# Optimization experiments

Hardware: AMD Instinct MI355X
Metric: run time of the kernel (lower is better)

## Reference

```python
import jax, jax.numpy as jnp
import numpy as np

N_NODES = 100000
N_EDGES = 1600000
N_GRAPHS = 256
IN_FEATS = 64
H_FEATS = 128
GN_EPS = 1e-5


def setup_inputs() -> dict:
    key = jax.random.key(0)
    ks = jax.random.split(key, 8)
    inputs = jax.random.normal(ks[0], (N_NODES, IN_FEATS), dtype=jnp.float32)
    edge_index = jax.random.randint(ks[1], (2, N_EDGES), 0, N_NODES, dtype=jnp.int64)
    batch = jnp.sort(jax.random.randint(ks[2], (N_NODES,), 0, N_GRAPHS, dtype=jnp.int64))
    edge_attr = jax.random.normal(ks[3], (N_EDGES, 8), dtype=jnp.float32)
    W1 = jax.random.normal(ks[4], (IN_FEATS, H_FEATS), dtype=jnp.float32) * 0.05
    W2 = jax.random.normal(ks[5], (H_FEATS, H_FEATS), dtype=jnp.float32) * 0.05
    W3 = jax.random.normal(ks[6], (H_FEATS, H_FEATS), dtype=jnp.float32) * 0.05
    return {
        'inputs': inputs, 'edge_index': edge_index, 'batch': batch, 'edge_attr': edge_attr,
        'W1': W1, 'b1': jnp.zeros((H_FEATS,), jnp.float32),
        'W2': W2, 'b2': jnp.zeros((H_FEATS,), jnp.float32),
        'W3': W3, 'b3': jnp.zeros((H_FEATS,), jnp.float32),
        'gn_weight': jnp.ones((H_FEATS,), jnp.float32),
        'gn_bias': jnp.zeros((H_FEATS,), jnp.float32),
        'gn_mean_scale': jnp.ones((H_FEATS,), jnp.float32),
    }


def reference(inputs, edge_index, batch, edge_attr, W1, b1, W2, b2, W3, b3, gn_weight, gn_bias, gn_mean_scale):
    src, dst = edge_index[0], edge_index[1]
    # GINConv with eps=0: h_i = MLP((1+eps)*x_i + sum_{j in N(i)} x_j)
    agg = jax.ops.segment_sum(inputs[src], dst, num_segments=N_NODES)
    h = inputs + agg
    # 3-layer ReLU MLP
    h = jax.nn.relu(h @ W1 + b1)
    h = jax.nn.relu(h @ W2 + b2)
    h = jax.nn.relu(h @ W3 + b3)
    # GraphNorm (per-graph mean shift with learnable mean_scale, then per-graph rms normalize)
    cnt = jnp.maximum(jax.ops.segment_sum(jnp.ones((N_NODES, 1), h.dtype), batch, num_segments=N_GRAPHS), 1.0)
    mean = jax.ops.segment_sum(h, batch, num_segments=N_GRAPHS) / cnt  # [G, H]
    out = h - mean[batch] * gn_mean_scale
    var = jax.ops.segment_sum(out * out, batch, num_segments=N_GRAPHS) / cnt  # [G, H]
    h_emb = out / jnp.sqrt(var[batch] + GN_EPS) * gn_weight + gn_bias
    # add_residue=False -> plain ReLU
    h_emb = jax.nn.relu(h_emb)
    # global max pool over each graph segment
    flat = jax.ops.segment_max(h_emb, batch, num_segments=N_GRAPHS)
    return (h_emb, flat, edge_index, edge_attr, batch)
```

## Files before the change

### kernel.cpp

```cpp
#include <hip/hip_runtime.h>
#include <math.h>

#define N_NODES 100000
#define N_EDGES 1600000
#define N_GRAPHS 256
#define IN_F 64
#define H_F 128
#define GN_EPS 1e-5f
#define PAD 32
#define NBINS 8
#define LCAP 512
#define BINCAP (1 << 18)
#define NSUB 16
#define SUBW 782
#define SBCAP 16384
#define MG 782
#define CPB 1612
#define CP_EI4 800000
#define CP_TOT 825000

typedef __attribute__((ext_vector_type(8))) short bf16x8;
typedef __attribute__((ext_vector_type(4))) float f32x4;

__device__ __forceinline__ float bf2f(unsigned short u) {
  return __uint_as_float(((unsigned int)u) << 16);
}
__device__ __forceinline__ unsigned short f2bf(float f) {
  unsigned int u = __float_as_uint(f);
  u += 0x7FFFu + ((u >> 16) & 1u);
  return (unsigned short)(u >> 16);
}
__device__ __forceinline__ int bsearch_batch(const int* __restrict__ batch, int target) {
  int lo = 0, hi = N_NODES;
  while (lo < hi) { int mid = (lo + hi) >> 1; if (batch[mid] < target) lo = mid + 1; else hi = mid; }
  return lo;
}

#define PREP_XH   1600000
#define PREP_GS   (PREP_XH + 16384)
#define PREP_WT   (PREP_GS + 40960)
#define PREP_CTR  (PREP_WT + 40)
#define PREP_FL   (PREP_CTR + 8192)
__global__ __launch_bounds__(256) void k_prep(
    const float4* __restrict__ xin, const float* __restrict__ W1,
    const float* __restrict__ W2, const float* __restrict__ W3,
    ushort4* __restrict__ xh4, float4* __restrict__ gsum4,
    unsigned short* __restrict__ wt, int4* __restrict__ ctr4,
    float4* __restrict__ flat4) {
  int i = blockIdx.x * 256 + threadIdx.x;
  if (i < PREP_XH) {
    float4 v = xin[i];
    ushort4 o;
    o.x = f2bf(v.x); o.y = f2bf(v.y); o.z = f2bf(v.z); o.w = f2bf(v.w);
    xh4[i] = o;
  } else if (i < PREP_GS) {
    gsum4[i - PREP_XH] = make_float4(0.f, 0.f, 0.f, 0.f);
  } else if (i < PREP_WT) {
    int j = i - PREP_GS;
    if (j < 8192) {
      int n = j >> 6, k = j & 63;
      wt[j] = f2bf(W1[(size_t)k * H_F + n]);
    } else if (j < 24576) {
      int jj = j - 8192;
      int n = jj >> 7, k = jj & 127;
      wt[j] = f2bf(W2[(size_t)k * H_F + n]);
    } else {
      int jj = j - 24576;
      int n = jj >> 7, k = jj & 127;
      wt[j] = f2bf(W3[(size_t)k * H_F + n]);
    }
  } else if (i < PREP_CTR) {
    ctr4[i - PREP_WT] = make_int4(0, 0, 0, 0);
  } else if (i < PREP_FL) {
    flat4[i - PREP_CTR] = make_float4(-INFINITY, -INFINITY, -INFINITY, -INFINITY);
  }
}

__global__ __launch_bounds__(256) void k_bin(
    const int* __restrict__ src, const int* __restrict__ dst,
    unsigned int* __restrict__ binBuf, int* __restrict__ gbc) {
  __shared__ unsigned int ebuf[NBINS][LCAP];
  __shared__ int lcnt[NBINS];
  __shared__ int lbase[NBINS];
  const int t = threadIdx.x;
  if (t < NBINS) lcnt[t] = 0;
  __syncthreads();
  for (int e0 = blockIdx.x * 256; e0 < N_EDGES; e0 += gridDim.x * 256) {
    int e = e0 + t;
    if (e < N_EDGES) {
      int s = src[e], d = dst[e];
      int b = d / 12500;
      int p = atomicAdd(&lcnt[b], 1);
      ebuf[b][p] = ((unsigned)(d - b * 12500) << 17) | (unsigned)s;
    }
    __syncthreads();
    if (t < NBINS && lcnt[t] >= 256) lbase[t] = atomicAdd(&gbc[t], lcnt[t]);
    __syncthreads();
#pragma unroll
    for (int b = 0; b < NBINS; ++b) {
      int c = lcnt[b];
      if (c >= 256) {
        unsigned int* gp = binBuf + (size_t)b * BINCAP + lbase[b];
        for (int i = t; i < c; i += 256) gp[i] = ebuf[b][i];
      }
    }
    __syncthreads();
    if (t < NBINS && lcnt[t] >= 256) lcnt[t] = 0;
    __syncthreads();
  }
  if (t < NBINS && lcnt[t] > 0) lbase[t] = atomicAdd(&gbc[t], lcnt[t]);
  __syncthreads();
#pragma unroll
  for (int b = 0; b < NBINS; ++b) {
    int c = lcnt[b];
    if (c > 0) {
      unsigned int* gp = binBuf + (size_t)b * BINCAP + lbase[b];
      for (int i = t; i < c; i += 256) gp[i] = ebuf[b][i];
    }
  }
}

__global__ __launch_bounds__(256) void k_bin2(
    const unsigned int* __restrict__ binBuf, const int* __restrict__ gbc,
    unsigned int* __restrict__ binBuf2, int* __restrict__ gbc2) {
  __shared__ unsigned int ebuf[NSUB][LCAP];
  __shared__ int lcnt[NSUB];
  __shared__ int lbase[NSUB];
  const int t = threadIdx.x;
  const int p = blockIdx.x & 7;
  const int blk = blockIdx.x >> 3;
  const int nb = gbc[p];
  const unsigned int* buf = binBuf + (size_t)p * BINCAP;
  if (t < NSUB) lcnt[t] = 0;
  __syncthreads();
  for (int i0 = blk * 256; i0 < nb; i0 += 32 * 256) {
    int i = i0 + t;
    if (i < nb) {
      unsigned int e = buf[i];
      int dloc = (int)(e >> 17);
      int sub = dloc / SUBW;
      int p2 = atomicAdd(&lcnt[sub], 1);
      ebuf[sub][p2] = ((unsigned)(dloc - sub * SUBW) << 17) | (e & 131071u);
    }
    __syncthreads();
    if (t < NSUB && lcnt[t] >= 256)
      lbase[t] = atomicAdd(&gbc2[p * NSUB + t], lcnt[t]);
    __syncthreads();
#pragma unroll
    for (int b = 0; b < NSUB; ++b) {
      int c = lcnt[b];
      if (c >= 256) {
        unsigned int* gp = binBuf2 + (size_t)(p * NSUB + b) * SBCAP + lbase[b];
        for (int i2 = t; i2 < c; i2 += 256) gp[i2] = ebuf[b][i2];
      }
    }
    __syncthreads();
    if (t < NSUB && lcnt[t] >= 256) lcnt[t] = 0;
    __syncthreads();
  }
  if (t < NSUB && lcnt[t] > 0)
    lbase[t] = atomicAdd(&gbc2[p * NSUB + t], lcnt[t]);
  __syncthreads();
#pragma unroll
  for (int b = 0; b < NSUB; ++b) {
    int c = lcnt[b];
    if (c > 0) {
      unsigned int* gp = binBuf2 + (size_t)(p * NSUB + b) * SBCAP + lbase[b];
      for (int i2 = t; i2 < c; i2 += 256) gp[i2] = ebuf[b][i2];
    }
  }
}

__global__ __launch_bounds__(256) void k_fill5(
    const unsigned int* __restrict__ binBuf2, const int* __restrict__ gbc2,
    int* __restrict__ csr, int* __restrict__ cnt,
    int* __restrict__ ovfc, int* __restrict__ ovf) {
  __shared__ int lcsr[SUBW * PAD];
  __shared__ int lcnt[SUBW];
  const int t = threadIdx.x;
  const int p = blockIdx.x & 7;
  const int sub = blockIdx.x >> 3;
  for (int j = t; j < SUBW; j += 256) lcnt[j] = 0;
  __syncthreads();
  const int n2 = gbc2[p * NSUB + sub];
  const unsigned int* buf = binBuf2 + (size_t)(p * NSUB + sub) * SBCAP;
  const int dbase = p * 12500 + sub * SUBW;
  for (int i = t; i < n2; i += 256) {
    unsigned int e = buf[i];
    int dloc2 = (int)(e >> 17);
    int s = (int)(e & 131071u);
    int pos = atomicAdd(&lcnt[dloc2], 1);
    if (pos < PAD) {
      lcsr[dloc2 * PAD + pos] = s;
    } else {
      int o = atomicAdd(ovfc, 1);
      ovf[2 * o] = s;
      ovf[2 * o + 1] = dbase + dloc2;
    }
  }
  __syncthreads();
  int rows = 12500 - sub * SUBW; if (rows > SUBW) rows = SUBW;
  int total4 = rows * (PAD / 4);
  int4* dst4 = (int4*)(csr + (size_t)dbase * PAD);
  const int4* src4 = (const int4*)lcsr;
  for (int i = t; i < total4; i += 256) dst4[i] = src4[i];
  for (int j = t; j < rows; j += 256)
    cnt[dbase + j] = lcnt[j];
}

__global__ __launch_bounds__(256) void k_gather(
    const unsigned short* __restrict__ xh, const int* __restrict__ csr,
    const int* __restrict__ cnt, unsigned short* __restrict__ xa,
    const int* __restrict__ ovfc, const int* __restrict__ ovf) {
  int wid = (blockIdx.x * 256 + threadIdx.x) >> 6;
  if (wid >= N_NODES) return;
  const int lane = threadIdx.x & 63;
  const int g = lane >> 4;
  const int fl = lane & 15;
  int rawdeg = cnt[wid];
  int deg = rawdeg > PAD ? PAD : rawdeg;
  int myE = csr[(size_t)wid * PAD + (lane & 31)];
  float s0 = 0.f, s1 = 0.f, s2 = 0.f, s3 = 0.f;
  int j = g;
  for (; j + 12 < deg; j += 16) {
    int sA = __shfl(myE, j);
    int sB = __shfl(myE, j + 4);
    int sC = __shfl(myE, j + 8);
    int sD = __shfl(myE, j + 12);
    ushort4 a = *(const ushort4*)&xh[(size_t)sA * IN_F + fl * 4];
    ushort4 b = *(const ushort4*)&xh[(size_t)sB * IN_F + fl * 4];
    ushort4 c = *(const ushort4*)&xh[(size_t)sC * IN_F + fl * 4];
    ushort4 d = *(const ushort4*)&xh[(size_t)sD * IN_F + fl * 4];
    s0 += bf2f(a.x) + bf2f(b.x) + bf2f(c.x) + bf2f(d.x);
    s1 += bf2f(a.y) + bf2f(b.y) + bf2f(c.y) + bf2f(d.y);
    s2 += bf2f(a.z) + bf2f(b.z) + bf2f(c.z) + bf2f(d.z);
    s3 += bf2f(a.w) + bf2f(b.w) + bf2f(c.w) + bf2f(d.w);
  }
  for (; j < deg; j += 4) {
    int sA = __shfl(myE, j);
    ushort4 a = *(const ushort4*)&xh[(size_t)sA * IN_F + fl * 4];
    s0 += bf2f(a.x); s1 += bf2f(a.y); s2 += bf2f(a.z); s3 += bf2f(a.w);
  }
  if (rawdeg > PAD && g == 0) {
    int n = *ovfc;
    for (int o = 0; o < n; ++o) {
      if (ovf[2 * o + 1] == wid) {
        int s = ovf[2 * o];
        ushort4 a = *(const ushort4*)&xh[(size_t)s * IN_F + fl * 4];
        s0 += bf2f(a.x); s1 += bf2f(a.y); s2 += bf2f(a.z); s3 += bf2f(a.w);
      }
    }
  }
  s0 += __shfl_xor(s0, 16); s1 += __shfl_xor(s1, 16);
  s2 += __shfl_xor(s2, 16); s3 += __shfl_xor(s3, 16);
  s0 += __shfl_xor(s0, 32); s1 += __shfl_xor(s1, 32);
  s2 += __shfl_xor(s2, 32); s3 += __shfl_xor(s3, 32);
  if (g == 0) {
    ushort4 self = *(const ushort4*)&xh[(size_t)wid * IN_F + fl * 4];
    s0 += bf2f(self.x); s1 += bf2f(self.y);
    s2 += bf2f(self.z); s3 += bf2f(self.w);
    ushort4 r;
    r.x = f2bf(s0); r.y = f2bf(s1); r.z = f2bf(s2); r.w = f2bf(s3);
    *(ushort4*)&xa[(size_t)wid * IN_F + fl * 4] = r;
  }
}

__global__ __launch_bounds__(512) void k_mlp(
    const unsigned short* __restrict__ xa,
    const unsigned short* __restrict__ wt1,
    const unsigned short* __restrict__ wt2,
    const unsigned short* __restrict__ wt3,
    const float* __restrict__ b1, const float* __restrict__ b2,
    const float* __restrict__ b3,
    unsigned short* __restrict__ h3,
    const int* __restrict__ batch,
    float* __restrict__ gsum, float* __restrict__ gsumq,
    const int4* __restrict__ ei4, const int4* __restrict__ bat4,
    float4* __restrict__ o_ei4, float4* __restrict__ o_b4) {
  __shared__ unsigned short sh[128 * 128];
  __shared__ float ssum[H_F], ssq[H_F];
  const int t = threadIdx.x;
  if (blockIdx.x >= MG) {
    int cb = blockIdx.x - MG;
    for (int i = cb * 512 + t; i < CP_TOT; i += CPB * 512) {
      if (i < CP_EI4) {
        int4 v = ei4[i];
        o_ei4[i] = make_float4((float)v.x, (float)v.y, (float)v.z, (float)v.w);
      } else {
        int j = i - CP_EI4;
        int4 v = bat4[j];
        o_b4[j] = make_float4((float)v.x, (float)v.y, (float)v.z, (float)v.w);
      }
    }
    return;
  }
  const int lane = t & 63;
  const int wv = t >> 6;
  const int row16 = lane & 15;
  const int kg = lane >> 4;
  const long blk0 = (long)blockIdx.x * 128;
  const int lr0 = (wv & 3) * 32;
  const int nb = (wv >> 2) * 4;
  f32x4 acc0[4], acc1[4];

  {
    long arow0 = blk0 + lr0 + row16;      if (arow0 > N_NODES - 1) arow0 = N_NODES - 1;
    long arow1 = blk0 + lr0 + 16 + row16; if (arow1 > N_NODES - 1) arow1 = N_NODES - 1;
    bf16x8 a0[2], a1[2];
    const unsigned short* ap0 = xa + arow0 * IN_F + kg * 8;
    const unsigned short* ap1 = xa + arow1 * IN_F + kg * 8;
#pragma unroll
    for (int s = 0; s < 2; ++s) {
      a0[s] = *(const bf16x8*)(ap0 + s * 32);
      a1[s] = *(const bf16x8*)(ap1 + s * 32);
    }
#pragma unroll
    for (int n = 0; n < 4; ++n) {
      acc0[n] = (f32x4){0.f, 0.f, 0.f, 0.f};
      acc1[n] = (f32x4){0.f, 0.f, 0.f, 0.f};
    }
#pragma unroll
    for (int n = 0; n < 4; ++n) {
      const unsigned short* wpn =
          wt1 + (size_t)((nb + n) * 16 + row16) * IN_F + kg * 8;
      bf16x8 b[2];
      b[0] = *(const bf16x8*)(wpn);
      b[1] = *(const bf16x8*)(wpn + 32);
      acc0[n] = __builtin_amdgcn_mfma_f32_16x16x32_bf16(a0[0], b[0], acc0[n], 0, 0, 0);
      acc0[n] = __builtin_amdgcn_mfma_f32_16x16x32_bf16(a0[1], b[1], acc0[n], 0, 0, 0);
      acc1[n] = __builtin_amdgcn_mfma_f32_16x16x32_bf16(a1[0], b[0], acc1[n], 0, 0, 0);
      acc1[n] = __builtin_amdgcn_mfma_f32_16x16x32_bf16(a1[1], b[1], acc1[n], 0, 0, 0);
    }
#pragma unroll
    for (int n = 0; n < 4; ++n) {
      int col = (nb + n) * 16 + row16;
      float bv = b1[col];
#pragma unroll
      for (int r = 0; r < 4; ++r) {
        int lrow0 = lr0 + kg * 4 + r;
        int lrow1 = lrow0 + 16;
        sh[lrow0 * 128 + (col ^ ((lrow0 & 7) << 3))] = f2bf(fmaxf(acc0[n][r] + bv, 0.f));
        sh[lrow1 * 128 + (col ^ ((lrow1 & 7) << 3))] = f2bf(fmaxf(acc1[n][r] + bv, 0.f));
      }
    }
  }
  __syncthreads();

  {
    const int lA0 = lr0 + row16, lA1 = lr0 + 16 + row16;
    bf16x8 a0[4], a1[4];
#pragma unroll
    for (int s = 0; s < 4; ++s) {
      int K0 = s * 32 + kg * 8;
      a0[s] = *(const bf16x8*)&sh[lA0 * 128 + (K0 ^ ((lA0 & 7) << 3))];
      a1[s] = *(const bf16x8*)&sh[lA1 * 128 + (K0 ^ ((lA1 & 7) << 3))];
    }
#pragma unroll
    for (int n = 0; n < 4; ++n) {
      acc0[n] = (f32x4){0.f, 0.f, 0.f, 0.f};
      acc1[n] = (f32x4){0.f, 0.f, 0.f, 0.f};
    }
#pragma unroll
    for (int n = 0; n < 4; ++n) {
      const unsigned short* wpn =
          wt2 + (size_t)((nb + n) * 16 + row16) * H_F + kg * 8;
      bf16x8 b[4];
#pragma unroll
      for (int s = 0; s < 4; ++s) b[s] = *(const bf16x8*)(wpn + s * 32);
#pragma unroll
      for (int s = 0; s < 4; ++s) {
        acc0[n] = __builtin_amdgcn_mfma_f32_16x16x32_bf16(a0[s], b[s], acc0[n], 0, 0, 0);
        acc1[n] = __builtin_amdgcn_mfma_f32_16x16x32_bf16(a1[s], b[s], acc1[n], 0, 0, 0);
      }
    }
    __syncthreads();
#pragma unroll
    for (int n = 0; n < 4; ++n) {
      int col = (nb + n) * 16 + row16;
      float bv = b2[col];
#pragma unroll
      for (int r = 0; r < 4; ++r) {
        int lrow0 = lr0 + kg * 4 + r;
        int lrow1 = lrow0 + 16;
        sh[lrow0 * 128 + (col ^ ((lrow0 & 7) << 3))] = f2bf(fmaxf(acc0[n][r] + bv, 0.f));
        sh[lrow1 * 128 + (col ^ ((lrow1 & 7) << 3))] = f2bf(fmaxf(acc1[n][r] + bv, 0.f));
      }
    }
  }
  __syncthreads();

  {
    const int lA0 = lr0 + row16, lA1 = lr0 + 16 + row16;
    bf16x8 a0[4], a1[4];
#pragma unroll
    for (int s = 0; s < 4; ++s) {
      int K0 = s * 32 + kg * 8;
      a0[s] = *(const bf16x8*)&sh[lA0 * 128 + (K0 ^ ((lA0 & 7) << 3))];
      a1[s] = *(const bf16x8*)&sh[lA1 * 128 + (K0 ^ ((lA1 & 7) << 3))];
    }
#pragma unroll
    for (int n = 0; n < 4; ++n) {
      acc0[n] = (f32x4){0.f, 0.f, 0.f, 0.f};
      acc1[n] = (f32x4){0.f, 0.f, 0.f, 0.f};
    }
#pragma unroll
    for (int n = 0; n < 4; ++n) {
      const unsigned short* wpn =
          wt3 + (size_t)((nb + n) * 16 + row16) * H_F + kg * 8;
      bf16x8 b[4];
#pragma unroll
      for (int s = 0; s < 4; ++s) b[s] = *(const bf16x8*)(wpn + s * 32);
#pragma unroll
      for (int s = 0; s < 4; ++s) {
        acc0[n] = __builtin_amdgcn_mfma_f32_16x16x32_bf16(a0[s], b[s], acc0[n], 0, 0, 0);
        acc1[n] = __builtin_amdgcn_mfma_f32_16x16x32_bf16(a1[s], b[s], acc1[n], 0, 0, 0);
      }
    }
#pragma unroll
    for (int n = 0; n < 4; ++n) {
      int col = (nb + n) * 16 + row16;
      float bv = b3[col];
#pragma unroll
      for (int r = 0; r < 4; ++r) {
        long row0 = blk0 + lr0 + kg * 4 + r;
        long row1 = row0 + 16;
        if (row0 < N_NODES)
          h3[row0 * H_F + col] = f2bf(fmaxf(acc0[n][r] + bv, 0.f));
        if (row1 < N_NODES)
          h3[row1 * H_F + col] = f2bf(fmaxf(acc1[n][r] + bv, 0.f));
      }
    }
    long lastrow = blk0 + 127; if (lastrow > N_NODES - 1) lastrow = N_NODES - 1;
    const int glo = batch[blk0];
    const int ghi = batch[lastrow];
    int br0[4], br1[4];
#pragma unroll
    for (int r = 0; r < 4; ++r) {
      long row0 = blk0 + lr0 + kg * 4 + r;
      long row1 = row0 + 16;
      br0[r] = (row0 < N_NODES) ? batch[row0] : -1;
      br1[r] = (row1 < N_NODES) ? batch[row1] : -1;
    }
    for (int g = glo; g <= ghi; ++g) {
      if (t < H_F) { ssum[t] = 0.f; ssq[t] = 0.f; }
      __syncthreads();
#pragma unroll
      for (int n = 0; n < 4; ++n) {
        int col = (nb + n) * 16 + row16;
        float bvn = b3[col];
        float sn = 0.f, qn = 0.f;
#pragma unroll
        for (int r = 0; r < 4; ++r) {
          if (br0[r] == g) { float f = fmaxf(acc0[n][r] + bvn, 0.f); sn += f; qn += f * f; }
          if (br1[r] == g) { float f = fmaxf(acc1[n][r] + bvn, 0.f); sn += f; qn += f * f; }
        }
        sn += __shfl_xor(sn, 16); qn += __shfl_xor(qn, 16);
        sn += __shfl_xor(sn, 32); qn += __shfl_xor(qn, 32);
        if (kg == 0) {
          atomicAdd(&ssum[col], sn);
          atomicAdd(&ssq[col], qn);
        }
      }
      __syncthreads();
      if (t < H_F) {
        unsafeAtomicAdd(&gsum[(size_t)g * H_F + t], ssum[t]);
        unsafeAtomicAdd(&gsumq[(size_t)g * H_F + t], ssq[t]);
      }
      __syncthreads();
    }
  }
}

__global__ __launch_bounds__(256) void k_apply2(
    const unsigned short* __restrict__ h3, const int* __restrict__ batch,
    const float* __restrict__ gsum, const float* __restrict__ gsumsq,
    const float* __restrict__ gms, const float* __restrict__ gw,
    const float* __restrict__ gb, float* __restrict__ hemb,
    float* __restrict__ flat) {
  const int t = threadIdx.x;
  const int rg = t >> 5, fq = t & 31;
  const int m0 = blockIdx.x * 32;
  const int r0 = m0 + rg * 4;
  const int c0 = fq * 4;
  const float4 bb = *(const float4*)&gb[c0];
  const float4 gm = *(const float4*)&gms[c0];
  const float4 gwv = *(const float4*)&gw[c0];
  const int glo = batch[m0], ghi = batch[m0 + 31];
  __shared__ int sb[2];
  __shared__ __align__(16) float4 mred[8][32];
  if (glo == ghi) {
    if (t < 2) sb[t] = bsearch_batch(batch, glo + t);
    __syncthreads();
    float c = fmaxf((float)(sb[1] - sb[0]), 1.0f);
    float4 S = *(const float4*)&gsum[(size_t)glo * H_F + c0];
    float4 Q = *(const float4*)&gsumsq[(size_t)glo * H_F + c0];
    float4 mm, ss;
    {
      float mean, ms, var;
      mean = S.x / c; ms = mean * gm.x; var = fmaxf(Q.x / c - 2.f * ms * mean + ms * ms, 0.f);
      mm.x = ms; ss.x = gwv.x * rsqrtf(var + GN_EPS);
      mean = S.y / c; ms = mean * gm.y; var = fmaxf(Q.y / c - 2.f * ms * mean + ms * ms, 0.f);
      mm.y = ms; ss.y = gwv.y * rsqrtf(var + GN_EPS);
      mean = S.z / c; ms = mean * gm.z; var = fmaxf(Q.z / c - 2.f * ms * mean + ms * ms, 0.f);
      mm.z = ms; ss.z = gwv.z * rsqrtf(var + GN_EPS);
      mean = S.w / c; ms = mean * gm.w; var = fmaxf(Q.w / c - 2.f * ms * mean + ms * ms, 0.f);
      mm.w = ms; ss.w = gwv.w * rsqrtf(var + GN_EPS);
    }
    float4 mx = {-INFINITY, -INFINITY, -INFINITY, -INFINITY};
#pragma unroll
    for (int i = 0; i < 4; ++i) {
      size_t idx = (size_t)(r0 + i) * H_F + c0;
      ushort4 u = *(const ushort4*)&h3[idx];
      float4 v;
      v.x = fmaxf((bf2f(u.x) - mm.x) * ss.x + bb.x, 0.f);
      v.y = fmaxf((bf2f(u.y) - mm.y) * ss.y + bb.y, 0.f);
      v.z = fmaxf((bf2f(u.z) - mm.z) * ss.z + bb.z, 0.f);
      v.w = fmaxf((bf2f(u.w) - mm.w) * ss.w + bb.w, 0.f);
      *(float4*)&hemb[idx] = v;
      mx.x = fmaxf(mx.x, v.x); mx.y = fmaxf(mx.y, v.y);
      mx.z = fmaxf(mx.z, v.z); mx.w = fmaxf(mx.w, v.w);
    }
    mred[rg][fq] = mx;
    __syncthreads();
    if (rg == 0) {
#pragma unroll
      for (int j = 1; j < 8; ++j) {
        float4 a = mred[j][fq];
        mx.x = fmaxf(mx.x, a.x); mx.y = fmaxf(mx.y, a.y);
        mx.z = fmaxf(mx.z, a.z); mx.w = fmaxf(mx.w, a.w);
      }
      int* pf = (int*)&flat[(size_t)glo * H_F + c0];
      atomicMax(pf + 0, __float_as_int(mx.x));
      atomicMax(pf + 1, __float_as_int(mx.y));
      atomicMax(pf + 2, __float_as_int(mx.z));
      atomicMax(pf + 3, __float_as_int(mx.w));
    }
  } else {
    int gcur = -1;
    float4 mm = {0,0,0,0}, ss = {0,0,0,0};
    float4 mx = {-INFINITY, -INFINITY, -INFINITY, -INFINITY};
#pragma unroll
    for (int i = 0; i < 4; ++i) {
      int g = batch[r0 + i];
      if (g != gcur) {
        if (gcur >= 0) {
          int* pf = (int*)&flat[(size_t)gcur * H_F + c0];
          atomicMax(pf + 0, __float_as_int(mx.x));
          atomicMax(pf + 1, __float_as_int(mx.y));
          atomicMax(pf + 2, __float_as_int(mx.z));
          atomicMax(pf + 3, __float_as_int(mx.w));
          mx = make_float4(-INFINITY, -INFINITY, -INFINITY, -INFINITY);
        }
        gcur = g;
        int lo = bsearch_batch(batch, g);
        int hi = bsearch_batch(batch, g + 1);
        float c = fmaxf((float)(hi - lo), 1.0f);
        float4 S = *(const float4*)&gsum[(size_t)g * H_F + c0];
        float4 Q = *(const float4*)&gsumsq[(size_t)g * H_F + c0];
        float mean, ms, var;
        mean = S.x / c; ms = mean * gm.x; var = fmaxf(Q.x / c - 2.f * ms * mean + ms * ms, 0.f);
        mm.x = ms; ss.x = gwv.x * rsqrtf(var + GN_EPS);
        mean = S.y / c; ms = mean * gm.y; var = fmaxf(Q.y / c - 2.f * ms * mean + ms * ms, 0.f);
        mm.y = ms; ss.y = gwv.y * rsqrtf(var + GN_EPS);
        mean = S.z / c; ms = mean * gm.z; var = fmaxf(Q.z / c - 2.f * ms * mean + ms * ms, 0.f);
        mm.z = ms; ss.z = gwv.z * rsqrtf(var + GN_EPS);
        mean = S.w / c; ms = mean * gm.w; var = fmaxf(Q.w / c - 2.f * ms * mean + ms * ms, 0.f);
        mm.w = ms; ss.w = gwv.w * rsqrtf(var + GN_EPS);
      }
      size_t idx = (size_t)(r0 + i) * H_F + c0;
      ushort4 u = *(const ushort4*)&h3[idx];
      float4 v;
      v.x = fmaxf((bf2f(u.x) - mm.x) * ss.x + bb.x, 0.f);
      v.y = fmaxf((bf2f(u.y) - mm.y) * ss.y + bb.y, 0.f);
      v.z = fmaxf((bf2f(u.z) - mm.z) * ss.z + bb.z, 0.f);
      v.w = fmaxf((bf2f(u.w) - mm.w) * ss.w + bb.w, 0.f);
      *(float4*)&hemb[idx] = v;
      mx.x = fmaxf(mx.x, v.x); mx.y = fmaxf(mx.y, v.y);
      mx.z = fmaxf(mx.z, v.z); mx.w = fmaxf(mx.w, v.w);
    }
    int* pf = (int*)&flat[(size_t)gcur * H_F + c0];
    atomicMax(pf + 0, __float_as_int(mx.x));
    atomicMax(pf + 1, __float_as_int(mx.y));
    atomicMax(pf + 2, __float_as_int(mx.z));
    atomicMax(pf + 3, __float_as_int(mx.w));
  }
}

__global__ __launch_bounds__(256) void k_copy_ea(
    const float4* __restrict__ ea4, float4* __restrict__ o_ea4, int n4) {
  int i = blockIdx.x * 256 + threadIdx.x;
  if (i < n4) o_ea4[i] = ea4[i];
}

extern "C" void kernel_launch(void* const* d_in, const int* in_sizes, int n_in,
                              void* d_out, int out_size, void* d_ws, size_t ws_size,
                              hipStream_t stream) {
  const float* inputs = (const float*)d_in[0];
  const int*   ei     = (const int*)d_in[1];
  const int*   batch  = (const int*)d_in[2];
  const float* eattr  = (const float*)d_in[3];
  const float* W1 = (const float*)d_in[4];
  const float* b1 = (const float*)d_in[5];
  const float* W2 = (const float*)d_in[6];
  const float* b2 = (const float*)d_in[7];
  const float* W3 = (const float*)d_in[8];
  const float* b3 = (const float*)d_in[9];
  const float* gw  = (const float*)d_in[10];
  const float* gb  = (const float*)d_in[11];
  const float* gms = (const float*)d_in[12];

  float* out = (float*)d_out;
  float* hemb  = out;
  float* flat  = out + 12800000;
  float* o_ei  = out + 12832768;
  float* o_ea  = out + 16032768;
  float* o_b   = out + 28832768;

  unsigned int*   binBuf  = (unsigned int*)hemb;
  unsigned int*   binBuf2 = (unsigned int*)(hemb + 2100000);
  unsigned short* xh = (unsigned short*)(hemb + 4200000);
  unsigned short* xa = (unsigned short*)(hemb + 7600000);
  int*            csr = (int*)o_ea;
  unsigned short* h3  = (unsigned short*)(o_ea + 6400000);
  float* gsum  = o_ea + 3200000;
  float* gsumq = o_ea + 3232768;
  unsigned short* wt  = (unsigned short*)(o_ea + 3265536);
  unsigned short* wt1 = wt;
  unsigned short* wt2 = wt + 8192;
  unsigned short* wt3 = wt + 24576;
  int*   cnt   = (int*)o_ei;
  int*   ovfc  = (int*)o_ei + 100000;
  int*   gbc   = (int*)o_ei + 100008;
  int*   gbc2  = (int*)o_ei + 100016;
  int*   ovf   = (int*)o_ei + 100160;

  k_prep<<<(PREP_FL + 255) / 256, 256, 0, stream>>>(
      (const float4*)inputs, W1, W2, W3, (ushort4*)xh, (float4*)gsum, wt,
      (int4*)ovfc, (float4*)flat);
  k_bin<<<512, 256, 0, stream>>>(ei, ei + N_EDGES, binBuf, gbc);
  k_bin2<<<256, 256, 0, stream>>>(binBuf, gbc, binBuf2, gbc2);
  k_fill5<<<NBINS * NSUB, 256, 0, stream>>>(binBuf2, gbc2, csr, cnt, ovfc, ovf);
  k_gather<<<(N_NODES * 64 + 255) / 256, 256, 0, stream>>>(xh, csr, cnt, xa, ovfc, ovf);
  k_mlp<<<MG + CPB, 512, 0, stream>>>(xa, wt1, wt2, wt3, b1, b2, b3, h3, batch,
                                      gsum, gsumq, (const int4*)ei,
                                      (const int4*)batch, (float4*)o_ei,
                                      (float4*)o_b);
  k_apply2<<<N_NODES / 32, 256, 0, stream>>>(h3, batch, gsum, gsumq, gms, gw, gb,
                                             hemb, flat);
  k_copy_ea<<<(N_EDGES * 2 + 255) / 256, 256, 0, stream>>>(
      (const float4*)eattr, (float4*)o_ea, N_EDGES * 2);
}
```

Before: 245.4 us.

## Move scratch to workspace and overlap output copies with gather and MLP

When the workspace is large enough, h3 moves into the workspace and the CSR count/overflow buffers move into the edge_attr output region. This frees the edge_index and batch output regions, so their int-to-float conversion can run in extra blocks of the gather kernel. The edge_attr copy then runs inside spare MLP blocks instead of a separate full-size kernel, and a small kernel afterwards copies only the window still used by gsum/weights. The aim is to hide output copy bandwidth behind compute kernels, at the cost of a more complex buffer aliasing scheme that depends on ws_size.

```diff
diff --git a/kernel.cpp b/kernel.cpp
--- a/kernel.cpp
+++ b/kernel.cpp
@@ -16,8 +16,13 @@
 #define SBCAP 16384
 #define MG 782
 #define CPB 1612
+#define GCB 25000
+#define GCPB 1000
 #define CP_EI4 800000
-#define CP_TOT 825000
+#define CP_EIB 825000
+#define EA_TOT4 3200000
+#define WIN_LO 800000
+#define WIN_HI 821504
 
 typedef __attribute__((ext_vector_type(8))) short bf16x8;
 typedef __attribute__((ext_vector_type(4))) float f32x4;
@@ -211,7 +216,24 @@
 __global__ __launch_bounds__(256) void k_gather(
     const unsigned short* __restrict__ xh, const int* __restrict__ csr,
     const int* __restrict__ cnt, unsigned short* __restrict__ xa,
-    const int* __restrict__ ovfc, const int* __restrict__ ovf) {
+    const int* __restrict__ ovfc, const int* __restrict__ ovf,
+    const int4* __restrict__ ei4, const int4* __restrict__ bat4,
+    float4* __restrict__ o_ei4, float4* __restrict__ o_b4) {
+  if (blockIdx.x >= GCB) {
+    int cb = blockIdx.x - GCB;
+    int stride = (gridDim.x - GCB) * 256;
+    for (int i = cb * 256 + threadIdx.x; i < CP_EIB; i += stride) {
+      if (i < CP_EI4) {
+        int4 v = ei4[i];
+        o_ei4[i] = make_float4((float)v.x, (float)v.y, (float)v.z, (float)v.w);
+      } else {
+        int j = i - CP_EI4;
+        int4 v = bat4[j];
+        o_b4[j] = make_float4((float)v.x, (float)v.y, (float)v.z, (float)v.w);
+      }
+    }
+    return;
+  }
   int wid = (blockIdx.x * 256 + threadIdx.x) >> 6;
   if (wid >= N_NODES) return;
   const int lane = threadIdx.x & 63;
@@ -276,20 +298,29 @@
     const int* __restrict__ batch,
     float* __restrict__ gsum, float* __restrict__ gsumq,
     const int4* __restrict__ ei4, const int4* __restrict__ bat4,
-    float4* __restrict__ o_ei4, float4* __restrict__ o_b4) {
+    const float4* __restrict__ ea4,
+    float4* __restrict__ o_ei4, float4* __restrict__ o_b4,
+    float4* __restrict__ o_ea4, int eaMode) {
   __shared__ unsigned short sh[128 * 128];
   __shared__ float ssum[H_F], ssq[H_F];
   const int t = threadIdx.x;
   if (blockIdx.x >= MG) {
     int cb = blockIdx.x - MG;
-    for (int i = cb * 512 + t; i < CP_TOT; i += CPB * 512) {
-      if (i < CP_EI4) {
-        int4 v = ei4[i];
-        o_ei4[i] = make_float4((float)v.x, (float)v.y, (float)v.z, (float)v.w);
-      } else {
-        int j = i - CP_EI4;
-        int4 v = bat4[j];
-        o_b4[j] = make_float4((float)v.x, (float)v.y, (float)v.z, (float)v.w);
+    if (eaMode) {
+      for (int i = cb * 512 + t; i < EA_TOT4; i += CPB * 512) {
+        if (i >= WIN_LO && i < WIN_HI) continue;
+        o_ea4[i] = ea4[i];
+      }
+    } else {
+      for (int i = cb * 512 + t; i < CP_EIB; i += CPB * 512) {
+        if (i < CP_EI4) {
+          int4 v = ei4[i];
+          o_ei4[i] = make_float4((float)v.x, (float)v.y, (float)v.z, (float)v.w);
+        } else {
+          int j = i - CP_EI4;
+          int4 v = bat4[j];
+          o_b4[j] = make_float4((float)v.x, (float)v.y, (float)v.z, (float)v.w);
+        }
       }
     }
     return;
@@ -586,6 +617,11 @@
   }
 }
 
+__global__ __launch_bounds__(256) void k_copy_win(
+    const float4* __restrict__ ea4, float4* __restrict__ o_ea4) {
+  int i = WIN_LO + blockIdx.x * 256 + threadIdx.x;
+  if (i < WIN_HI) o_ea4[i] = ea4[i];
+}
 __global__ __launch_bounds__(256) void k_copy_ea(
     const float4* __restrict__ ea4, float4* __restrict__ o_ea4, int n4) {
   int i = blockIdx.x * 256 + threadIdx.x;
@@ -621,18 +657,31 @@
   unsigned short* xh = (unsigned short*)(hemb + 4200000);
   unsigned short* xa = (unsigned short*)(hemb + 7600000);
   int*            csr = (int*)o_ea;
-  unsigned short* h3  = (unsigned short*)(o_ea + 6400000);
   float* gsum  = o_ea + 3200000;
   float* gsumq = o_ea + 3232768;
   unsigned short* wt  = (unsigned short*)(o_ea + 3265536);
   unsigned short* wt1 = wt;
   unsigned short* wt2 = wt + 8192;
   unsigned short* wt3 = wt + 24576;
-  int*   cnt   = (int*)o_ei;
-  int*   ovfc  = (int*)o_ei + 100000;
-  int*   gbc   = (int*)o_ei + 100008;
-  int*   gbc2  = (int*)o_ei + 100016;
-  int*   ovf   = (int*)o_ei + 100160;
+
+  const bool big = ws_size >= (size_t)25600000;
+  unsigned short* h3;
+  int *cnt, *ovfc, *gbc, *gbc2, *ovf;
+  if (big) {
+    h3   = (unsigned short*)d_ws;
+    cnt  = (int*)o_ea + 3400000;
+    ovfc = (int*)o_ea + 3500000;
+    gbc  = ovfc + 8;
+    gbc2 = ovfc + 16;
+    ovf  = ovfc + 160;
+  } else {
+    h3   = (unsigned short*)(o_ea + 6400000);
+    cnt  = (int*)o_ei;
+    ovfc = (int*)o_ei + 100000;
+    gbc  = ovfc + 8;
+    gbc2 = ovfc + 16;
+    ovf  = ovfc + 160;
+  }
 
   k_prep<<<(PREP_FL + 255) / 256, 256, 0, stream>>>(
       (const float4*)inputs, W1, W2, W3, (ushort4*)xh, (float4*)gsum, wt,
@@ -640,13 +689,25 @@
   k_bin<<<512, 256, 0, stream>>>(ei, ei + N_EDGES, binBuf, gbc);
   k_bin2<<<256, 256, 0, stream>>>(binBuf, gbc, binBuf2, gbc2);
   k_fill5<<<NBINS * NSUB, 256, 0, stream>>>(binBuf2, gbc2, csr, cnt, ovfc, ovf);
-  k_gather<<<(N_NODES * 64 + 255) / 256, 256, 0, stream>>>(xh, csr, cnt, xa, ovfc, ovf);
-  k_mlp<<<MG + CPB, 512, 0, stream>>>(xa, wt1, wt2, wt3, b1, b2, b3, h3, batch,
-                                      gsum, gsumq, (const int4*)ei,
-                                      (const int4*)batch, (float4*)o_ei,
-                                      (float4*)o_b);
-  k_apply2<<<N_NODES / 32, 256, 0, stream>>>(h3, batch, gsum, gsumq, gms, gw, gb,
-                                             hemb, flat);
-  k_copy_ea<<<(N_EDGES * 2 + 255) / 256, 256, 0, stream>>>(
-      (const float4*)eattr, (float4*)o_ea, N_EDGES * 2);
-}
+  if (big) {
+    k_gather<<<GCB + GCPB, 256, 0, stream>>>(xh, csr, cnt, xa, ovfc, ovf,
+        (const int4*)ei, (const int4*)batch, (float4*)o_ei, (float4*)o_b);
+    k_mlp<<<MG + CPB, 512, 0, stream>>>(xa, wt1, wt2, wt3, b1, b2, b3, h3, batch,
+        gsum, gsumq, (const int4*)ei, (const int4*)batch, (const float4*)eattr,
+        (float4*)o_ei, (float4*)o_b, (float4*)o_ea, 1);
+    k_apply2<<<N_NODES / 32, 256, 0, stream>>>(h3, batch, gsum, gsumq, gms, gw, gb,
+                                               hemb, flat);
+    k_copy_win<<<(WIN_HI - WIN_LO + 255) / 256, 256, 0, stream>>>(
+        (const float4*)eattr, (float4*)o_ea);
+  } else {
+    k_gather<<<GCB, 256, 0, stream>>>(xh, csr, cnt, xa, ovfc, ovf,
+        (const int4*)ei, (const int4*)batch, (float4*)o_ei, (float4*)o_b);
+    k_mlp<<<MG + CPB, 512, 0, stream>>>(xa, wt1, wt2, wt3, b1, b2, b3, h3, batch,
+        gsum, gsumq, (const int4*)ei, (const int4*)batch, (const float4*)eattr,
+        (float4*)o_ei, (float4*)o_b, (float4*)o_ea, 0);
+    k_apply2<<<N_NODES / 32, 256, 0, stream>>>(h3, batch, gsum, gsumq, gms, gw, gb,
+                                               hemb, flat);
+    k_copy_ea<<<(N_EDGES * 2 + 255) / 256, 256, 0, stream>>>(
+        (const float4*)eattr, (float4*)o_ea, N_EDGES * 2);
+  }
+}
```

Result: faster. 234.1 us (-4.6%).
